# Kernel tuning notes

Hardware: AMD Instinct MI355X
Metric: run time of the kernel (lower is better)

The kernel has to match this reference:

```python
import jax, jax.numpy as jnp
import numpy as np

H = 12      # heads
P = 4       # dim_point
LN_EPS = 1e-5


def setup_inputs() -> dict:
    key = jax.random.key(0)
    ks = jax.random.split(key, 24)
    B, N, C, Dp, E = 1, 2048, 768, 128, 49152
    D3 = H * P * 3

    def w(k, shape, s=0.02):
        return jax.random.normal(k, shape, jnp.float32) * s

    inp = {
        'single': jax.random.normal(ks[0], (B, N, C), jnp.float32),
        'edge_feat': jax.random.normal(ks[1], (E, Dp), jnp.float32),
        'rot': jax.random.normal(ks[2], (B, N, 3, 3), jnp.float32),
        'trans': jax.random.normal(ks[3], (B, N, 3), jnp.float32),
        'Wq': w(ks[4], (C, C)), 'bq': jnp.zeros((C,), jnp.float32),
        'Wk': w(ks[5], (C, C)), 'bk': jnp.zeros((C,), jnp.float32),
        'Wv': w(ks[6], (C, C)), 'bv': jnp.zeros((C,), jnp.float32),
        'Wpb': w(ks[7], (Dp, H)), 'bpb': jnp.zeros((H,), jnp.float32),
        'Wqp': w(ks[8], (C, D3)), 'bqp': jnp.zeros((D3,), jnp.float32),
        'Wkp': w(ks[9], (C, D3)), 'bkp': jnp.zeros((D3,), jnp.float32),
        'Wvp': w(ks[10], (C, D3)), 'bvp': jnp.zeros((D3,), jnp.float32),
        'Wo': w(ks[11], (C, C)), 'bo': jnp.zeros((C,), jnp.float32),
        'Wpo': w(ks[12], (D3, C)), 'bpo': jnp.zeros((C,), jnp.float32),
        'gamma': jnp.ones((C,), jnp.float32),
        'beta': jnp.zeros((C,), jnp.float32),
        'edge_index': jax.random.randint(ks[13], (2, E), 0, B * N, jnp.int64),
    }
    return inp


def reference(single, edge_feat, rot, trans,
              Wq, bq, Wk, bk, Wv, bv, Wpb, bpb,
              Wqp, bqp, Wkp, bkp, Wvp, bvp,
              Wo, bo, Wpo, bpo, gamma, beta, edge_index):
    B, N, C = single.shape
    C_h = C // H
    scale = C_h ** (-0.5)

    # scalar q/k/v: [B,N,H,C_h]
    q = (single @ Wq + bq).reshape(B, N, H, C_h)
    k = (single @ Wk + bk).reshape(B, N, H, C_h)
    v = (single @ Wv + bv).reshape(B, N, H, C_h)

    # sparse pair bias scatter -> dense [B,H,N,N], symmetrized
    pbs = edge_feat @ Wpb + bpb                       # [E,H]
    src, dst = edge_index[0], edge_index[1]
    b_idx, ls, ld = src // N, src % N, dst % N
    pair_bias = jnp.zeros((B, H, N, N), single.dtype).at[b_idx, :, ls, ld].set(pbs)
    pair_bias = pair_bias + jnp.swapaxes(pair_bias, -1, -2)

    # point q/k/v in global frame: [B,N,H,P,3]
    def to_global(W, b):
        pts = (single @ W + b).reshape(B, N, H, P, 3)
        return jnp.einsum('bnhpd,bnde->bnhpe', pts, rot) + trans[:, :, None, None, :]

    q_pts = to_global(Wqp, bqp)
    k_pts = to_global(Wkp, bkp)
    v_pts = to_global(Wvp, bvp)

    q2 = jnp.sum(q_pts ** 2, axis=(3, 4))             # [B,N,H]
    k2 = jnp.sum(k_pts ** 2, axis=(3, 4))             # [B,N,H]

    # logits (blockwise loop in torch == full computation; math identical)
    scalar_logits = jnp.einsum('bqhc,bkhc->bhqk', q, k) * scale
    qk_pts = jnp.einsum('bqhpd,bkhpd->bhqk', q_pts, k_pts)
    point_logits = -0.5 * (jnp.transpose(q2, (0, 2, 1))[:, :, :, None]
                           + jnp.transpose(k2, (0, 2, 1))[:, :, None, :]
                           - 2.0 * qk_pts) * scale
    logits = scalar_logits + point_logits + pair_bias
    attn = jax.nn.softmax(logits, axis=-1)            # [B,H,N,N]

    attn_scalar = jnp.einsum('bhqk,bkhc->bqhc', attn, v).reshape(B, N, C)
    attn_points = jnp.einsum('bhqk,bkhpd->bqhpd', attn, v_pts).reshape(B, N, H * P * 3)

    out = (attn_scalar @ Wo + bo) + (attn_points @ Wpo + bpo)
    x = single + out
    mu = jnp.mean(x, axis=-1, keepdims=True)
    var = jnp.mean((x - mu) ** 2, axis=-1, keepdims=True)
    return (x - mu) * jax.lax.rsqrt(var + LN_EPS) * gamma + beta
```

## Files before the change

### kernel.cpp

```cpp
#include <hip/hip_runtime.h>

#define NRES 2048
#define NH 12
#define CDIM 768
#define NCVT 16
#define QKELEMS (NH * NRES * 96)
#define LOG2E 1.44269504f

typedef unsigned short u16;
typedef __bf16 bf16x8 __attribute__((ext_vector_type(8)));
typedef float f32x4 __attribute__((ext_vector_type(4)));

#define MFMA16(a,b,c) __builtin_amdgcn_mfma_f32_16x16x32_bf16(a,b,c,0,0,0)

__device__ __forceinline__ float bf2f(u16 u){
  unsigned int x = ((unsigned int)u) << 16;
  return __builtin_bit_cast(float, x);
}
__device__ __forceinline__ u16 f2bf(float f){
  unsigned int x = __builtin_bit_cast(unsigned int, f);
  x += 0x7fffu + ((x >> 16) & 1u);
  return (u16)(x >> 16);
}

__global__ void detect_kernel(const unsigned int* __restrict__ g,
                              const int* __restrict__ ei, int* __restrict__ flags)
{
  if (threadIdx.x == 0 && blockIdx.x == 0) {
    flags[0] = (g[0] == 0x3F800000u) ? 1 : 0;
    int allz = 1;
    for (int i = 1; i < 64; i += 2) allz &= (ei[i] == 0);
    flags[1] = allz;
  }
}

struct CvtDesc {
  const void* src[NCVT];
  void* dst[NCVT];
  int n[NCVT];
  int f32dst[NCVT];
  int nblk[NCVT];
};

__global__ __launch_bounds__(256) void cvt_kernel(CvtDesc d, const int* __restrict__ flags)
{
  int b = blockIdx.x, id = 0;
  while (id < NCVT - 1 && b >= d.nblk[id]) { b -= d.nblk[id]; id++; }
  int n = d.n[id];
  int base = (b * 256 + threadIdx.x) * 4;
  if (base >= n) return;
  int srcf32 = flags[0];
  const void* s = d.src[id];
  void* o = d.dst[id];
  int f32o = d.f32dst[id];
  #pragma unroll
  for (int k = 0; k < 4; k++) {
    int i = base + k;
    if (i >= n) break;
    float v = srcf32 ? ((const float*)s)[i] : bf2f(((const u16*)s)[i]);
    if (f32o) ((float*)o)[i] = v;
    else      ((u16*)o)[i] = f2bf(v);
  }
}

struct TDesc { const void* src; u16* dst; int R, C, ostride, ooff, rtiles, ctiles; };
struct TTable { TDesc d[9]; };

__global__ __launch_bounds__(256) void tcvt_kernel(TTable tt, const int* __restrict__ flags)
{
  TDesc d = tt.d[blockIdx.y];
  int tr = blockIdx.x % d.rtiles, tc = blockIdx.x / d.rtiles;
  if (tc >= d.ctiles) return;
  int srcf32 = flags[0];
  __shared__ float tile[32][33];
  int r0 = tr * 32, c0 = tc * 32;
  int x = threadIdx.x, y = threadIdx.y;
  #pragma unroll
  for (int i = 0; i < 32; i += 8) {
    int r = r0 + y + i, c = c0 + x;
    float v = 0.f;
    if (r < d.R && c < d.C) {
      long idx = (long)r * d.C + c;
      v = srcf32 ? ((const float*)d.src)[idx] : bf2f(((const u16*)d.src)[idx]);
    }
    tile[y + i][x] = v;
  }
  __syncthreads();
  #pragma unroll
  for (int i = 0; i < 32; i += 8) {
    int c = c0 + y + i, r = r0 + x;
    if (c < d.C && r < d.R) d.dst[(long)c * d.ostride + d.ooff + r] = f2bf(tile[x][y + i]);
  }
}

__global__ __launch_bounds__(256) void transpose_k(
    const u16* __restrict__ in, u16* __restrict__ out,
    int R, int Cc, int ostride, int ooff, long inBatch, long outBatch)
{
  in  += (long)blockIdx.z * inBatch;
  out += (long)blockIdx.z * outBatch;
  __shared__ u16 tile[32][33];
  int r0 = blockIdx.x * 32, c0 = blockIdx.y * 32;
  int tc = threadIdx.x, tr = threadIdx.y;
  #pragma unroll
  for (int i = 0; i < 32; i += 8) {
    int r = r0 + tr + i, c = c0 + tc;
    tile[tr + i][tc] = (r < R && c < Cc) ? in[(long)r * Cc + c] : (u16)0;
  }
  __syncthreads();
  #pragma unroll
  for (int i = 0; i < 32; i += 8) {
    int c = c0 + tr + i, r = r0 + tc;
    if (c < Cc && r < R) out[(long)c * ostride + ooff + r] = tile[tc][tr + i];
  }
}

__global__ __launch_bounds__(256) void scatter_kernel(
    const int* __restrict__ ei, const int* __restrict__ flags,
    int* __restrict__ winner, int* __restrict__ winnerT, int E)
{
  int e = blockIdx.x * 256 + threadIdx.x;
  if (e >= E) return;
  int s, d;
  if (flags[1]) { s = ei[2 * e]; d = ei[2 * (E + e)]; }
  else          { s = ei[e];     d = ei[E + e]; }
  int ls = s % NRES, ld = d % NRES;
  atomicMax(&winner[(long)ls * NRES + ld], e);
  atomicMax(&winnerT[(long)ld * NRES + ls], e);
}

__global__ __launch_bounds__(256) void bias_fill(
    const int* __restrict__ winner, const int* __restrict__ winnerT,
    const float* __restrict__ pbs, unsigned int* __restrict__ Bias)
{
  long idx = ((long)blockIdx.x * 256 + threadIdx.x) * 2;
  int2 w1 = *(const int2*)&winner[idx];
  int2 w2 = *(const int2*)&winnerT[idx];
  float b0[NH], b1[NH];
  #pragma unroll
  for (int h = 0; h < NH; h++) { b0[h] = 0.f; b1[h] = 0.f; }
  int ws0[2] = { w1.x, w2.x };
  int ws1[2] = { w1.y, w2.y };
  #pragma unroll
  for (int t = 0; t < 2; t++) {
    if (ws0[t] >= 0) {
      const float* p = &pbs[(long)ws0[t] * NH];
      #pragma unroll
      for (int h = 0; h < NH; h++) b0[h] += p[h];
    }
    if (ws1[t] >= 0) {
      const float* p = &pbs[(long)ws1[t] * NH];
      #pragma unroll
      for (int h = 0; h < NH; h++) b1[h] += p[h];
    }
  }
  long half = idx >> 1;
  #pragma unroll
  for (int h = 0; h < NH; h++) {
    unsigned int pack = (unsigned int)f2bf(b0[h] * LOG2E) | ((unsigned int)f2bf(b1[h] * LOG2E) << 16);
    Bias[(long)h * (NRES * (long)NRES / 2) + half] = pack;
  }
}

__global__ __launch_bounds__(256) void gemm64(
    const u16* __restrict__ A, int lda, const u16* __restrict__ BT, int ldb,
    const u16* __restrict__ bias1, const u16* __restrict__ bias2,
    const float* __restrict__ residf,
    int Nout, int Ktot, int mode, void* __restrict__ outp)
{
  __shared__ u16 As[64][40];
  __shared__ u16 Bs[64][40];
  int tid = threadIdx.x;
  int wave = tid >> 6, lane = tid & 63;
  int wr = (wave >> 1) * 32, wc = (wave & 1) * 32;
  int row0 = blockIdx.x * 64, col0 = blockIdx.y * 64;
  int rsub = lane & 15, kb8 = (lane >> 4) * 8;
  int sr = tid >> 2, sseg = tid & 3;
  f32x4 acc[2][2] = {};
  for (int k0 = 0; k0 < Ktot; k0 += 32) {
    __syncthreads();
    uint4 av = *(const uint4*)&A[(long)(row0 + sr) * lda + k0 + sseg * 8];
    *(uint4*)&As[sr][sseg * 8] = av;
    uint4 bv = {0u, 0u, 0u, 0u};
    if (col0 + sr < Nout) bv = *(const uint4*)&BT[(long)(col0 + sr) * ldb + k0 + sseg * 8];
    *(uint4*)&Bs[sr][sseg * 8] = bv;
    __syncthreads();
    bf16x8 af0 = *(const bf16x8*)&As[wr + rsub][kb8];
    bf16x8 af1 = *(const bf16x8*)&As[wr + 16 + rsub][kb8];
    bf16x8 bt0 = *(const bf16x8*)&Bs[wc + rsub][kb8];
    bf16x8 bt1 = *(const bf16x8*)&Bs[wc + 16 + rsub][kb8];
    acc[0][0] = MFMA16(af0, bt0, acc[0][0]);
    acc[0][1] = MFMA16(af0, bt1, acc[0][1]);
    acc[1][0] = MFMA16(af1, bt0, acc[1][0]);
    acc[1][1] = MFMA16(af1, bt1, acc[1][1]);
  }
  #pragma unroll
  for (int fm = 0; fm < 2; fm++)
  #pragma unroll
  for (int fn = 0; fn < 2; fn++)
  #pragma unroll
  for (int r = 0; r < 4; r++) {
    int row = row0 + wr + fm * 16 + (lane >> 4) * 4 + r;
    int col = col0 + wc + fn * 16 + rsub;
    if (col >= Nout) continue;
    float v = acc[fm][fn][r];
    if (mode == 1) {
      ((float*)outp)[(long)row * Nout + col] = v + bf2f(bias1[col]);
    } else if (mode == 2) {
      v += bf2f(bias1[col]) + bf2f(bias2[col]) + residf[(long)row * CDIM + col];
      ((float*)outp)[(long)row * CDIM + col] = v;
    } else {
      int seg = col / 768;
      int lc = col - seg * 768;
      int hh = lc >> 6, c6 = lc & 63;
      float sc = (seg == 0) ? (0.125f * LOG2E) : 1.0f;
      v = (v + bf2f(bias1[col])) * sc;
      u16* qb = (u16*)outp;
      u16* dst;
      if (seg < 2) dst = qb + (long)seg * QKELEMS + (long)hh * NRES * 96 + (long)row * 96 + c6;
      else         dst = qb + 2L * QKELEMS + (long)hh * NRES * 80 + (long)row * 80 + c6;
      *dst = f2bf(v);
    }
  }
}

__global__ __launch_bounds__(256) void point_transform(
    const float* __restrict__ Tmp3, const float* __restrict__ rot, const float* __restrict__ trans,
    u16* __restrict__ Qext, float* __restrict__ q2s, float* __restrict__ k2s)
{
  int t = blockIdx.x * 256 + threadIdx.x;
  if (t >= NRES * NH) return;
  int n = t / NH, h = t - n * NH;
  float R[9], T3[3];
  #pragma unroll
  for (int i = 0; i < 9; i++) R[i] = rot[n * 9 + i];
  #pragma unroll
  for (int i = 0; i < 3; i++) T3[i] = trans[n * 3 + i];
  #pragma unroll
  for (int seg = 0; seg < 3; seg++) {
    const float* lp = &Tmp3[(long)n * 432 + seg * 144 + h * 12];
    u16* dst;
    float scale;
    int npad;
    if (seg < 2) { dst = Qext + (long)seg * QKELEMS + (long)h * NRES * 96 + (long)n * 96 + 64; scale = (seg == 0) ? 0.125f * LOG2E : 1.0f; npad = 20; }
    else         { dst = Qext + 2L * QKELEMS + (long)h * NRES * 80 + (long)n * 80 + 64; scale = 1.0f; npad = 4; }
    float g2 = 0.f;
    #pragma unroll
    for (int pp = 0; pp < 4; pp++) {
      float a = lp[pp * 3], b = lp[pp * 3 + 1], c = lp[pp * 3 + 2];
      #pragma unroll
      for (int e = 0; e < 3; e++) {
        float g = a * R[e] + b * R[3 + e] + c * R[6 + e] + T3[e];
        g2 += g * g;
        dst[pp * 3 + e] = f2bf(scale * g);
      }
    }
    for (int p = 0; p < npad; p++) dst[12 + p] = 0;
    if (seg == 0) q2s[(long)h * NRES + n] = 0.0625f * LOG2E * g2;
    if (seg == 1) k2s[(long)h * NRES + n] = 0.0625f * LOG2E * g2;
  }
}

__global__ __launch_bounds__(256) void attn_pass1(
    const u16* __restrict__ Qext, const u16* __restrict__ VextT,
    const float* __restrict__ q2s, const float* __restrict__ k2s,
    const u16* __restrict__ Bias, float* __restrict__ Part)
{
  int h = blockIdx.y;
  int part = blockIdx.z;
  int q0 = blockIdx.x * 64;
  int tid = threadIdx.x, wave = tid >> 6, lane = tid & 63;
  int rsub = lane & 15, kb8 = (lane >> 4) * 8;
  __shared__ u16 Ks[32][104];
  __shared__ u16 Vs[80][40];
  __shared__ u16 Bs64[64][40];
  __shared__ u16 Ps[4][16][40];

  const u16* Qh = Qext + (long)h * NRES * 96;
  const u16* Kh = Qext + (long)QKELEMS + (long)h * NRES * 96;
  const u16* VTh = VextT + (long)h * 80 * NRES;
  const float* k2h = k2s + (long)h * NRES;
  const u16* BiasH = Bias + (long)h * NRES * NRES;

  int qrow = q0 + wave * 16;
  bf16x8 qf[3];
  #pragma unroll
  for (int f = 0; f < 3; f++)
    qf[f] = *(const bf16x8*)&Qh[(long)(qrow + rsub) * 96 + f * 32 + kb8];
  int crow = qrow + (lane >> 4) * 4;
  int lrow0 = wave * 16 + (lane >> 4) * 4;
  float q2r[4];
  #pragma unroll
  for (int r = 0; r < 4; r++) q2r[r] = q2s[(long)h * NRES + crow + r];
  float lsum[4] = {0.f, 0.f, 0.f, 0.f};
  f32x4 acc[5] = {};

  int jbase = part * 512;
  int krr = tid / 6, kcc = (tid - krr * 6) * 16;
  int vrr = tid >> 2, vcc = (tid & 3) * 8;
  uint4 kr0, kr1, vr0, vr1, br;

  auto LOAD = [&](int t) {
    int j0 = jbase + t * 32;
    if (tid < 192) {
      kr0 = *(const uint4*)&Kh[(long)(j0 + krr) * 96 + kcc];
      kr1 = *(const uint4*)&Kh[(long)(j0 + krr) * 96 + kcc + 8];
    }
    vr0 = *(const uint4*)&VTh[(long)vrr * NRES + j0 + vcc];
    if (tid < 64)
      vr1 = *(const uint4*)&VTh[(long)(64 + vrr) * NRES + j0 + vcc];
    br = *(const uint4*)&BiasH[(long)(q0 + vrr) * NRES + j0 + vcc];
  };

  LOAD(0);
  for (int t = 0; t < 16; t++) {
    int j0 = jbase + t * 32;
    __syncthreads();
    if (tid < 192) {
      *(uint4*)&Ks[krr][kcc]     = kr0;
      *(uint4*)&Ks[krr][kcc + 8] = kr1;
    }
    *(uint4*)&Vs[vrr][vcc] = vr0;
    if (tid < 64) *(uint4*)&Vs[64 + vrr][vcc] = vr1;
    *(uint4*)&Bs64[vrr][vcc] = br;
    __syncthreads();
    if (t < 15) LOAD(t + 1);

    f32x4 s[2];
    #pragma unroll
    for (int fn = 0; fn < 2; fn++) {
      f32x4 sv = {0.f, 0.f, 0.f, 0.f};
      #pragma unroll
      for (int f = 0; f < 3; f++) {
        bf16x8 kf = *(const bf16x8*)&Ks[fn * 16 + rsub][f * 32 + kb8];
        sv = MFMA16(qf[f], kf, sv);
      }
      s[fn] = sv;
    }
    #pragma unroll
    for (int fn = 0; fn < 2; fn++) {
      float k2v = k2h[j0 + fn * 16 + rsub];
      #pragma unroll
      for (int r = 0; r < 4; r++) {
        float b = bf2f(Bs64[lrow0 + r][fn * 16 + rsub]);
        float p = exp2f(s[fn][r] - q2r[r] - k2v + b);
        lsum[r] += p;
        Ps[wave][(lane >> 4) * 4 + r][fn * 16 + rsub] = f2bf(p);
      }
    }
    asm volatile("s_waitcnt lgkmcnt(0)" ::: "memory");
    __builtin_amdgcn_sched_barrier(0);
    bf16x8 pa = *(const bf16x8*)&Ps[wave][rsub][kb8];
    #pragma unroll
    for (int ff = 0; ff < 5; ff++) {
      bf16x8 vf = *(const bf16x8*)&Vs[ff * 16 + rsub][kb8];
      acc[ff] = MFMA16(pa, vf, acc[ff]);
    }
  }
  #pragma unroll
  for (int d = 1; d < 16; d <<= 1)
    #pragma unroll
    for (int r = 0; r < 4; r++) lsum[r] += __shfl_xor(lsum[r], d, 16);
  #pragma unroll
  for (int r = 0; r < 4; r++) {
    long basep = ((long)(part * NH + h) * NRES + (crow + r)) * 84;
    #pragma unroll
    for (int ff = 0; ff < 5; ff++)
      Part[basep + ff * 16 + rsub] = acc[ff][r];
    if (rsub == 0) Part[basep + 80] = lsum[r];
  }
}

__global__ __launch_bounds__(256) void attn_pass2(
    const float* __restrict__ Part, u16* __restrict__ ASP)
{
  int gid = blockIdx.x * 256 + threadIdx.x;
  int c = gid % 80;
  int pr = gid / 80;
  int h = pr / NRES, row = pr - h * NRES;
  float num = 0.f, den = 0.f;
  #pragma unroll
  for (int p = 0; p < 4; p++) {
    long basep = ((long)(p * NH + h) * NRES + row) * 84;
    num += Part[basep + c];
    den += Part[basep + 80];
  }
  float v = num / den;
  if (c < 64)      ASP[(long)row * 928 + h * 64 + c] = f2bf(v);
  else if (c < 76) ASP[(long)row * 928 + 768 + h * 12 + (c - 64)] = f2bf(v);
}

__global__ __launch_bounds__(256) void ln_kernel(
    const float* __restrict__ X, const float* __restrict__ gamma,
    const float* __restrict__ beta, const int* __restrict__ flags, void* __restrict__ out)
{
  int row = blockIdx.x;
  const float* x = &X[(long)row * CDIM];
  float s = 0.f, s2 = 0.f;
  for (int c = threadIdx.x; c < CDIM; c += 256) { float v = x[c]; s += v; s2 += v * v; }
  #pragma unroll
  for (int d = 1; d < 64; d <<= 1) { s += __shfl_xor(s, d, 64); s2 += __shfl_xor(s2, d, 64); }
  __shared__ float red[2][4];
  int wave = threadIdx.x >> 6, lane = threadIdx.x & 63;
  if (lane == 0) { red[0][wave] = s; red[1][wave] = s2; }
  __syncthreads();
  s = red[0][0] + red[0][1] + red[0][2] + red[0][3];
  s2 = red[1][0] + red[1][1] + red[1][2] + red[1][3];
  float mu = s * (1.f / CDIM);
  float var = s2 * (1.f / CDIM) - mu * mu;
  float rstd = rsqrtf(var + 1e-5f);
  int f32o = flags[0];
  for (int c = threadIdx.x; c < CDIM; c += 256) {
    float v = (x[c] - mu) * rstd * gamma[c] + beta[c];
    if (f32o) ((float*)out)[(long)row * CDIM + c] = v;
    else      ((u16*)out)[(long)row * CDIM + c] = f2bf(v);
  }
}

extern "C" void kernel_launch(void* const* d_in, const int* in_sizes, int n_in,
                              void* d_out, int out_size, void* d_ws, size_t ws_size,
                              hipStream_t stream)
{
  const void* single = d_in[0];
  const void* edge_feat = d_in[1];
  const void* rot = d_in[2];
  const void* trans = d_in[3];
  const void* Wq = d_in[4];  const void* bq = d_in[5];
  const void* Wk = d_in[6];  const void* bk = d_in[7];
  const void* Wv = d_in[8];  const void* bv = d_in[9];
  const void* Wpb = d_in[10]; const void* bpb = d_in[11];
  const void* Wqp = d_in[12]; const void* bqp = d_in[13];
  const void* Wkp = d_in[14]; const void* bkp = d_in[15];
  const void* Wvp = d_in[16]; const void* bvp = d_in[17];
  const void* Wo = d_in[18];  const void* bo = d_in[19];
  const void* Wpo = d_in[20]; const void* bpo = d_in[21];
  const void* gamma = d_in[22];
  const void* beta = d_in[23];
  const int* edge_index = (const int*)d_in[24];
  int E = in_sizes[24] / 2;

  char* base = (char*)d_ws;
  size_t off = 0;
  auto alloc = [&](size_t bytes) -> char* {
    char* r = base + off;
    off = (off + bytes + 255) & ~(size_t)255;
    return r;
  };
  int*   flags  = (int*)  alloc(256);
  int*   winner = (int*)  alloc((size_t)NRES * NRES * 4);
  int*   winnerT= (int*)  alloc((size_t)NRES * NRES * 4);
  u16*   Bias   = (u16*)  alloc((size_t)NH * NRES * NRES * 2);
  float* pbs    = (float*)alloc((size_t)E * NH * 4);
  float* Part   = (float*)winner;
  u16*   Qext   = (u16*)  alloc((size_t)QKELEMS * 2);
  u16*   Kext   = (u16*)  alloc((size_t)QKELEMS * 2);
  u16*   Vext   = (u16*)  alloc((size_t)NH * NRES * 80 * 2);
  u16*   VextT  = (u16*)  alloc((size_t)NH * 80 * NRES * 2);
  float* q2s    = (float*)alloc((size_t)NH * NRES * 4);
  float* k2s    = (float*)alloc((size_t)NH * NRES * 4);
  float* Tmp3   = (float*)alloc((size_t)NRES * 432 * 4);
  u16*   ASP    = (u16*)  alloc((size_t)NRES * 928 * 2);
  float* X      = (float*)alloc((size_t)NRES * CDIM * 4);
  u16* WqkvT = (u16*)alloc((size_t)2304 * 768 * 2);
  u16* WqkpT = (u16*)alloc((size_t)432 * 768 * 2);
  u16* WpbT  = (u16*)alloc((size_t)12 * 128 * 2);
  u16* WcatT = (u16*)alloc((size_t)768 * 928 * 2);
  u16*   single_bf  = (u16*)  alloc((size_t)NRES * 768 * 2);
  float* single_f32 = (float*)alloc((size_t)NRES * 768 * 4);
  u16*   ef_bf      = (u16*)  alloc((size_t)E * 128 * 2);
  float* rot_f      = (float*)alloc((size_t)NRES * 9 * 4);
  float* trans_f    = (float*)alloc((size_t)NRES * 3 * 4);
  u16* bqkv   = (u16*)alloc(2304*2);
  u16* bpb_bf = (u16*)alloc(12*2);
  u16* bqkp   = (u16*)alloc(432*2);
  u16* bo_bf  = (u16*)alloc(768*2);
  u16* bpo_bf = (u16*)alloc(768*2);
  float* gamma_f = (float*)alloc(768*4);
  float* beta_f  = (float*)alloc(768*4);

  hipMemsetAsync(winner,  0xFF, (size_t)NRES * NRES * 4, stream);
  hipMemsetAsync(winnerT, 0xFF, (size_t)NRES * NRES * 4, stream);
  hipMemsetAsync(ASP,  0, (size_t)NRES * 928 * 2, stream);
  hipMemsetAsync(WcatT,0, (size_t)768 * 928 * 2, stream);

  detect_kernel<<<1, 64, 0, stream>>>((const unsigned int*)gamma, edge_index, flags);

  CvtDesc cd;
  const void* srcs[NCVT] = { single, single, edge_feat, rot, trans,
    bq, bk, bv, bpb, bqp, bkp, bvp, bo, bpo, gamma, beta };
  void* dsts[NCVT] = { single_bf, single_f32, ef_bf, rot_f, trans_f,
    bqkv, bqkv + 768, bqkv + 1536, bpb_bf, bqkp, bqkp + 144, bqkp + 288,
    bo_bf, bpo_bf, gamma_f, beta_f };
  int ns[NCVT] = { NRES*768, NRES*768, E*128, NRES*9, NRES*3,
    768, 768, 768, 12, 144, 144, 144, 768, 768, 768, 768 };
  int f32d[NCVT] = { 0, 1, 0, 1, 1,
    0, 0, 0, 0, 0, 0, 0, 0, 0, 1, 1 };
  int totblk = 0;
  for (int i = 0; i < NCVT; i++) {
    cd.src[i]=srcs[i]; cd.dst[i]=dsts[i]; cd.n[i]=ns[i]; cd.f32dst[i]=f32d[i];
    cd.nblk[i] = (ns[i] + 1023) / 1024; totblk += cd.nblk[i];
  }
  cvt_kernel<<<totblk, 256, 0, stream>>>(cd, flags);

  TTable tt;
  auto setT = [&](int i, const void* s, u16* d, int R, int C, int ostride, int ooff) {
    tt.d[i] = TDesc{ s, d, R, C, ostride, ooff, (R + 31) / 32, (C + 31) / 32 };
  };
  setT(0, Wq,  WqkvT,             768, 768, 768, 0);
  setT(1, Wk,  WqkvT + 768*768,   768, 768, 768, 0);
  setT(2, Wv,  WqkvT + 2*768*768, 768, 768, 768, 0);
  setT(3, Wqp, WqkpT,             768, 144, 768, 0);
  setT(4, Wkp, WqkpT + 144*768,   768, 144, 768, 0);
  setT(5, Wvp, WqkpT + 288*768,   768, 144, 768, 0);
  setT(6, Wpb, WpbT,              128, 12,  128, 0);
  setT(7, Wo,  WcatT,             768, 768, 928, 0);
  setT(8, Wpo, WcatT,             144, 768, 928, 768);
  tcvt_kernel<<<dim3(576, 9), dim3(32, 8), 0, stream>>>(tt, flags);

  gemm64<<<dim3(E/64, 1), 256, 0, stream>>>(ef_bf, 128, WpbT, 128, bpb_bf, nullptr, nullptr, 12, 128, 1, pbs);
  scatter_kernel<<<(E + 255) / 256, 256, 0, stream>>>(edge_index, flags, winner, winnerT, E);
  bias_fill<<<(NRES * NRES / 2 + 255) / 256, 256, 0, stream>>>(winner, winnerT, pbs, (unsigned int*)Bias);

  gemm64<<<dim3(32, 36), 256, 0, stream>>>(single_bf, 768, WqkvT, 768, bqkv, nullptr, nullptr, 2304, 768, 3, Qext);
  gemm64<<<dim3(32, 7), 256, 0, stream>>>(single_bf, 768, WqkpT, 768, bqkp, nullptr, nullptr, 432, 768, 1, Tmp3);
  point_transform<<<(NRES * NH + 255) / 256, 256, 0, stream>>>(Tmp3, rot_f, trans_f, Qext, q2s, k2s);

  transpose_k<<<dim3(64,3,12), dim3(32,8), 0, stream>>>(Vext, VextT, NRES, 80, NRES, 0,
                                                        (long)NRES * 80, (long)80 * NRES);

  attn_pass1<<<dim3(32, 12, 4), 256, 0, stream>>>(Qext, VextT, q2s, k2s, Bias, Part);
  attn_pass2<<<(NRES * NH * 80) / 256, 256, 0, stream>>>(Part, ASP);

  gemm64<<<dim3(32, 12), 256, 0, stream>>>(ASP, 928, WcatT, 928, bo_bf, bpo_bf, single_f32, 768, 928, 2, X);

  ln_kernel<<<NRES, 256, 0, stream>>>(X, gamma_f, beta_f, flags, (u16*)d_out);
}
```

Baseline: 230.8 us.

## Fuse point projection into QKV GEMM and double-buffer attention prefetch

Result: faster. 213.0 us (-7.7%).

```diff
diff --git a/kernel.cpp b/kernel.cpp
--- a/kernel.cpp
+++ b/kernel.cpp
@@ -210,16 +210,20 @@
       v += bf2f(bias1[col]) + bf2f(bias2[col]) + residf[(long)row * CDIM + col];
       ((float*)outp)[(long)row * CDIM + col] = v;
     } else {
-      int seg = col / 768;
-      int lc = col - seg * 768;
-      int hh = lc >> 6, c6 = lc & 63;
-      float sc = (seg == 0) ? (0.125f * LOG2E) : 1.0f;
-      v = (v + bf2f(bias1[col])) * sc;
-      u16* qb = (u16*)outp;
-      u16* dst;
-      if (seg < 2) dst = qb + (long)seg * QKELEMS + (long)hh * NRES * 96 + (long)row * 96 + c6;
-      else         dst = qb + 2L * QKELEMS + (long)hh * NRES * 80 + (long)row * 80 + c6;
-      *dst = f2bf(v);
+      if (col < 2304) {
+        int seg = col / 768;
+        int lc = col - seg * 768;
+        int hh = lc >> 6, c6 = lc & 63;
+        float sc = (seg == 0) ? (0.125f * LOG2E) : 1.0f;
+        v = (v + bf2f(bias1[col])) * sc;
+        u16* qb = (u16*)outp;
+        u16* dst;
+        if (seg < 2) dst = qb + (long)seg * QKELEMS + (long)hh * NRES * 96 + (long)row * 96 + c6;
+        else         dst = qb + 2L * QKELEMS + (long)hh * NRES * 80 + (long)row * 80 + c6;
+        *dst = f2bf(v);
+      } else {
+        ((float*)residf)[(long)row * 432 + (col - 2304)] = v + bf2f(bias1[col]);
+      }
     }
   }
 }
@@ -298,65 +302,83 @@
   int jbase = part * 512;
   int krr = tid / 6, kcc = (tid - krr * 6) * 16;
   int vrr = tid >> 2, vcc = (tid & 3) * 8;
-  uint4 kr0, kr1, vr0, vr1, br;
-
-  auto LOAD = [&](int t) {
-    int j0 = jbase + t * 32;
-    if (tid < 192) {
-      kr0 = *(const uint4*)&Kh[(long)(j0 + krr) * 96 + kcc];
-      kr1 = *(const uint4*)&Kh[(long)(j0 + krr) * 96 + kcc + 8];
-    }
-    vr0 = *(const uint4*)&VTh[(long)vrr * NRES + j0 + vcc];
-    if (tid < 64)
-      vr1 = *(const uint4*)&VTh[(long)(64 + vrr) * NRES + j0 + vcc];
-    br = *(const uint4*)&BiasH[(long)(q0 + vrr) * NRES + j0 + vcc];
-  };
-
-  LOAD(0);
-  for (int t = 0; t < 16; t++) {
-    int j0 = jbase + t * 32;
+  uint4 kr0A, kr1A, vr0A, vr1A, brA;
+  uint4 kr0B, kr1B, vr0B, vr1B, brB;
+
+#define LOADSET(K0,K1,V0,V1,BR,T) do {                                         \
+    int j0_ = jbase + (T) * 32;                                                \
+    if (tid < 192) {                                                           \
+      K0 = *(const uint4*)&Kh[(long)(j0_ + krr) * 96 + kcc];                   \
+      K1 = *(const uint4*)&Kh[(long)(j0_ + krr) * 96 + kcc + 8];               \
+    }                                                                          \
+    V0 = *(const uint4*)&VTh[(long)vrr * NRES + j0_ + vcc];                    \
+    if (tid < 64)                                                              \
+      V1 = *(const uint4*)&VTh[(long)(64 + vrr) * NRES + j0_ + vcc];           \
+    BR = *(const uint4*)&BiasH[(long)(q0 + vrr) * NRES + j0_ + vcc];           \
+  } while (0)
+
+#define WRITESET(K0,K1,V0,V1,BR) do {                                          \
+    if (tid < 192) {                                                           \
+      *(uint4*)&Ks[krr][kcc]     = K0;                                         \
+      *(uint4*)&Ks[krr][kcc + 8] = K1;                                         \
+    }                                                                          \
+    *(uint4*)&Vs[vrr][vcc] = V0;                                               \
+    if (tid < 64) *(uint4*)&Vs[64 + vrr][vcc] = V1;                            \
+    *(uint4*)&Bs64[vrr][vcc] = BR;                                             \
+  } while (0)
+
+#define COMPUTE(T) do {                                                        \
+    int j0_ = jbase + (T) * 32;                                                \
+    f32x4 s[2];                                                                \
+    _Pragma("unroll")                                                          \
+    for (int fn = 0; fn < 2; fn++) {                                           \
+      f32x4 sv = {0.f, 0.f, 0.f, 0.f};                                         \
+      _Pragma("unroll")                                                        \
+      for (int f = 0; f < 3; f++) {                                            \
+        bf16x8 kf = *(const bf16x8*)&Ks[fn * 16 + rsub][f * 32 + kb8];         \
+        sv = MFMA16(qf[f], kf, sv);                                            \
+      }                                                                        \
+      s[fn] = sv;                                                              \
+    }                                                                          \
+    _Pragma("unroll")                                                          \
+    for (int fn = 0; fn < 2; fn++) {                                           \
+      float k2v = k2h[j0_ + fn * 16 + rsub];                                   \
+      _Pragma("unroll")                                                        \
+      for (int r = 0; r < 4; r++) {                                            \
+        float b = bf2f(Bs64[lrow0 + r][fn * 16 + rsub]);                       \
+        float p = exp2f(s[fn][r] - q2r[r] - k2v + b);                          \
+        lsum[r] += p;                                                          \
+        Ps[wave][(lane >> 4) * 4 + r][fn * 16 + rsub] = f2bf(p);               \
+      }                                                                        \
+    }                                                                          \
+    asm volatile("s_waitcnt lgkmcnt(0)" ::: "memory");                         \
+    __builtin_amdgcn_sched_barrier(0);                                         \
+    bf16x8 pa = *(const bf16x8*)&Ps[wave][rsub][kb8];                          \
+    _Pragma("unroll")                                                          \
+    for (int ff = 0; ff < 5; ff++) {                                           \
+      bf16x8 vf = *(const bf16x8*)&Vs[ff * 16 + rsub][kb8];                    \
+      acc[ff] = MFMA16(pa, vf, acc[ff]);                                       \
+    }                                                                          \
+  } while (0)
+
+  LOADSET(kr0A, kr1A, vr0A, vr1A, brA, 0);
+  LOADSET(kr0B, kr1B, vr0B, vr1B, brB, 1);
+  for (int t = 0; t < 16; t += 2) {
     __syncthreads();
-    if (tid < 192) {
-      *(uint4*)&Ks[krr][kcc]     = kr0;
-      *(uint4*)&Ks[krr][kcc + 8] = kr1;
-    }
-    *(uint4*)&Vs[vrr][vcc] = vr0;
-    if (tid < 64) *(uint4*)&Vs[64 + vrr][vcc] = vr1;
-    *(uint4*)&Bs64[vrr][vcc] = br;
+    WRITESET(kr0A, kr1A, vr0A, vr1A, brA);
     __syncthreads();
-    if (t < 15) LOAD(t + 1);
-
-    f32x4 s[2];
-    #pragma unroll
-    for (int fn = 0; fn < 2; fn++) {
-      f32x4 sv = {0.f, 0.f, 0.f, 0.f};
-      #pragma unroll
-      for (int f = 0; f < 3; f++) {
-        bf16x8 kf = *(const bf16x8*)&Ks[fn * 16 + rsub][f * 32 + kb8];
-        sv = MFMA16(qf[f], kf, sv);
-      }
-      s[fn] = sv;
-    }
-    #pragma unroll
-    for (int fn = 0; fn < 2; fn++) {
-      float k2v = k2h[j0 + fn * 16 + rsub];
-      #pragma unroll
-      for (int r = 0; r < 4; r++) {
-        float b = bf2f(Bs64[lrow0 + r][fn * 16 + rsub]);
-        float p = exp2f(s[fn][r] - q2r[r] - k2v + b);
-        lsum[r] += p;
-        Ps[wave][(lane >> 4) * 4 + r][fn * 16 + rsub] = f2bf(p);
-      }
-    }
-    asm volatile("s_waitcnt lgkmcnt(0)" ::: "memory");
-    __builtin_amdgcn_sched_barrier(0);
-    bf16x8 pa = *(const bf16x8*)&Ps[wave][rsub][kb8];
-    #pragma unroll
-    for (int ff = 0; ff < 5; ff++) {
-      bf16x8 vf = *(const bf16x8*)&Vs[ff * 16 + rsub][kb8];
-      acc[ff] = MFMA16(pa, vf, acc[ff]);
-    }
-  }
+    if (t + 2 < 16) LOADSET(kr0A, kr1A, vr0A, vr1A, brA, t + 2);
+    COMPUTE(t);
+    __syncthreads();
+    WRITESET(kr0B, kr1B, vr0B, vr1B, brB);
+    __syncthreads();
+    if (t + 3 < 16) LOADSET(kr0B, kr1B, vr0B, vr1B, brB, t + 3);
+    COMPUTE(t + 1);
+  }
+#undef LOADSET
+#undef WRITESET
+#undef COMPUTE
+
   #pragma unroll
   for (int d = 1; d < 16; d <<= 1)
     #pragma unroll
@@ -461,8 +483,7 @@
   float* Tmp3   = (float*)alloc((size_t)NRES * 432 * 4);
   u16*   ASP    = (u16*)  alloc((size_t)NRES * 928 * 2);
   float* X      = (float*)alloc((size_t)NRES * CDIM * 4);
-  u16* WqkvT = (u16*)alloc((size_t)2304 * 768 * 2);
-  u16* WqkpT = (u16*)alloc((size_t)432 * 768 * 2);
+  u16* WqkvT = (u16*)alloc((size_t)2736 * 768 * 2);
   u16* WpbT  = (u16*)alloc((size_t)12 * 128 * 2);
   u16* WcatT = (u16*)alloc((size_t)768 * 928 * 2);
   u16*   single_bf  = (u16*)  alloc((size_t)NRES * 768 * 2);
@@ -470,18 +491,15 @@
   u16*   ef_bf      = (u16*)  alloc((size_t)E * 128 * 2);
   float* rot_f      = (float*)alloc((size_t)NRES * 9 * 4);
   float* trans_f    = (float*)alloc((size_t)NRES * 3 * 4);
-  u16* bqkv   = (u16*)alloc(2304*2);
+  u16* bqkvp  = (u16*)alloc(2736*2);
   u16* bpb_bf = (u16*)alloc(12*2);
-  u16* bqkp   = (u16*)alloc(432*2);
   u16* bo_bf  = (u16*)alloc(768*2);
   u16* bpo_bf = (u16*)alloc(768*2);
   float* gamma_f = (float*)alloc(768*4);
   float* beta_f  = (float*)alloc(768*4);
 
-  hipMemsetAsync(winner,  0xFF, (size_t)NRES * NRES * 4, stream);
-  hipMemsetAsync(winnerT, 0xFF, (size_t)NRES * NRES * 4, stream);
-  hipMemsetAsync(ASP,  0, (size_t)NRES * 928 * 2, stream);
-  hipMemsetAsync(WcatT,0, (size_t)768 * 928 * 2, stream);
+  hipMemsetAsync(winner, 0xFF, (size_t)NRES * NRES * 8, stream);
+  hipMemsetAsync(WcatT, 0, (size_t)768 * 928 * 2, stream);
 
   detect_kernel<<<1, 64, 0, stream>>>((const unsigned int*)gamma, edge_index, flags);
 
@@ -489,7 +507,7 @@
   const void* srcs[NCVT] = { single, single, edge_feat, rot, trans,
     bq, bk, bv, bpb, bqp, bkp, bvp, bo, bpo, gamma, beta };
   void* dsts[NCVT] = { single_bf, single_f32, ef_bf, rot_f, trans_f,
-    bqkv, bqkv + 768, bqkv + 1536, bpb_bf, bqkp, bqkp + 144, bqkp + 288,
+    bqkvp, bqkvp + 768, bqkvp + 1536, bpb_bf, bqkvp + 2304, bqkvp + 2448, bqkvp + 2592,
     bo_bf, bpo_bf, gamma_f, beta_f };
   int ns[NCVT] = { NRES*768, NRES*768, E*128, NRES*9, NRES*3,
     768, 768, 768, 12, 144, 144, 144, 768, 768, 768, 768 };
@@ -509,9 +527,9 @@
   setT(0, Wq,  WqkvT,             768, 768, 768, 0);
   setT(1, Wk,  WqkvT + 768*768,   768, 768, 768, 0);
   setT(2, Wv,  WqkvT + 2*768*768, 768, 768, 768, 0);
-  setT(3, Wqp, WqkpT,             768, 144, 768, 0);
-  setT(4, Wkp, WqkpT + 144*768,   768, 144, 768, 0);
-  setT(5, Wvp, WqkpT + 288*768,   768, 144, 768, 0);
+  setT(3, Wqp, WqkvT + 2304*768,  768, 144, 768, 0);
+  setT(4, Wkp, WqkvT + 2448*768,  768, 144, 768, 0);
+  setT(5, Wvp, WqkvT + 2592*768,  768, 144, 768, 0);
   setT(6, Wpb, WpbT,              128, 12,  128, 0);
   setT(7, Wo,  WcatT,             768, 768, 928, 0);
   setT(8, Wpo, WcatT,             144, 768, 928, 768);
@@ -521,8 +539,7 @@
   scatter_kernel<<<(E + 255) / 256, 256, 0, stream>>>(edge_index, flags, winner, winnerT, E);
   bias_fill<<<(NRES * NRES / 2 + 255) / 256, 256, 0, stream>>>(winner, winnerT, pbs, (unsigned int*)Bias);
 
-  gemm64<<<dim3(32, 36), 256, 0, stream>>>(single_bf, 768, WqkvT, 768, bqkv, nullptr, nullptr, 2304, 768, 3, Qext);
-  gemm64<<<dim3(32, 7), 256, 0, stream>>>(single_bf, 768, WqkpT, 768, bqkp, nullptr, nullptr, 432, 768, 1, Tmp3);
+  gemm64<<<dim3(32, 43), 256, 0, stream>>>(single_bf, 768, WqkvT, 768, bqkvp, nullptr, Tmp3, 2736, 768, 3, Qext);
   point_transform<<<(NRES * NH + 255) / 256, 256, 0, stream>>>(Tmp3, rot_f, trans_f, Qext, q2s, k2s);
 
   transpose_k<<<dim3(64,3,12), dim3(32,8), 0, stream>>>(Vext, VextT, NRES, 80, NRES, 0,
```

## Store pair bias as 8-bit float, fuse point GEMM, fold row sums into MFMA

Applied to the files above, without the earlier changes.

Result: faster. 223.0 us (-3.4%).

```diff
diff --git a/kernel.cpp b/kernel.cpp
--- a/kernel.cpp
+++ b/kernel.cpp
@@ -8,6 +8,7 @@
 #define LOG2E 1.44269504f
 
 typedef unsigned short u16;
+typedef unsigned char u8;
 typedef __bf16 bf16x8 __attribute__((ext_vector_type(8)));
 typedef float f32x4 __attribute__((ext_vector_type(4)));
 
@@ -21,6 +22,28 @@
   unsigned int x = __builtin_bit_cast(unsigned int, f);
   x += 0x7fffu + ((x >> 16) & 1u);
   return (u16)(x >> 16);
+}
+
+__device__ __forceinline__ unsigned int enc8(float f){
+  if (f == 0.f) return 0u;
+  unsigned int bits = __builtin_bit_cast(unsigned int, f);
+  unsigned int s = (bits >> 24) & 0x80u;
+  unsigned int a = bits & 0x7fffffffu;
+  if (a >= 0x3C800000u) {
+    a += 0x0007FFFFu + ((a >> 20) & 1u);
+    if (a > 0x43E00000u) a = 0x43E00000u;
+    return s | (((a >> 23) - 120u) << 3) | ((a >> 20) & 7u);
+  }
+  float av = __builtin_bit_cast(float, a);
+  unsigned int q = (unsigned int)(av * 512.f + 0.5f);
+  if (q > 7u) return s | 0x08u;
+  return s | q;
+}
+__device__ __forceinline__ float dec8(unsigned int b){
+  unsigned int e = (b >> 3) & 15u, m = b & 7u;
+  float v = (e == 0) ? (float)m * 0.001953125f
+                     : __builtin_bit_cast(float, ((e + 120u) << 23) | (m << 20));
+  return (b & 0x80u) ? -v : v;
 }
 
 __global__ void detect_kernel(const unsigned int* __restrict__ g,
@@ -131,34 +154,39 @@
 
 __global__ __launch_bounds__(256) void bias_fill(
     const int* __restrict__ winner, const int* __restrict__ winnerT,
-    const float* __restrict__ pbs, unsigned int* __restrict__ Bias)
-{
-  long idx = ((long)blockIdx.x * 256 + threadIdx.x) * 2;
-  int2 w1 = *(const int2*)&winner[idx];
-  int2 w2 = *(const int2*)&winnerT[idx];
-  float b0[NH], b1[NH];
-  #pragma unroll
-  for (int h = 0; h < NH; h++) { b0[h] = 0.f; b1[h] = 0.f; }
-  int ws0[2] = { w1.x, w2.x };
-  int ws1[2] = { w1.y, w2.y };
-  #pragma unroll
-  for (int t = 0; t < 2; t++) {
-    if (ws0[t] >= 0) {
-      const float* p = &pbs[(long)ws0[t] * NH];
+    const float* __restrict__ pbs, unsigned int* __restrict__ Bias8)
+{
+  long idx = ((long)blockIdx.x * 256 + threadIdx.x) * 4;
+  int4 w1 = *(const int4*)&winner[idx];
+  int4 w2 = *(const int4*)&winnerT[idx];
+  float b[4][NH];
+  #pragma unroll
+  for (int c = 0; c < 4; c++)
+    #pragma unroll
+    for (int h = 0; h < NH; h++) b[c][h] = 0.f;
+  int wa[4] = { w1.x, w1.y, w1.z, w1.w };
+  int wb[4] = { w2.x, w2.y, w2.z, w2.w };
+  #pragma unroll
+  for (int c = 0; c < 4; c++) {
+    if (wa[c] >= 0) {
+      const float* p = &pbs[(long)wa[c] * NH];
       #pragma unroll
-      for (int h = 0; h < NH; h++) b0[h] += p[h];
-    }
-    if (ws1[t] >= 0) {
-      const float* p = &pbs[(long)ws1[t] * NH];
+      for (int h = 0; h < NH; h++) b[c][h] += p[h];
+    }
+    if (wb[c] >= 0) {
+      const float* p = &pbs[(long)wb[c] * NH];
       #pragma unroll
-      for (int h = 0; h < NH; h++) b1[h] += p[h];
-    }
-  }
-  long half = idx >> 1;
+      for (int h = 0; h < NH; h++) b[c][h] += p[h];
+    }
+  }
+  long quarter = idx >> 2;
   #pragma unroll
   for (int h = 0; h < NH; h++) {
-    unsigned int pack = (unsigned int)f2bf(b0[h] * LOG2E) | ((unsigned int)f2bf(b1[h] * LOG2E) << 16);
-    Bias[(long)h * (NRES * (long)NRES / 2) + half] = pack;
+    unsigned int pack = enc8(b[0][h] * LOG2E)
+                      | (enc8(b[1][h] * LOG2E) << 8)
+                      | (enc8(b[2][h] * LOG2E) << 16)
+                      | (enc8(b[3][h] * LOG2E) << 24);
+    Bias8[(long)h * (NRES * (long)NRES / 4) + quarter] = pack;
   }
 }
 
@@ -210,16 +238,20 @@
       v += bf2f(bias1[col]) + bf2f(bias2[col]) + residf[(long)row * CDIM + col];
       ((float*)outp)[(long)row * CDIM + col] = v;
     } else {
-      int seg = col / 768;
-      int lc = col - seg * 768;
-      int hh = lc >> 6, c6 = lc & 63;
-      float sc = (seg == 0) ? (0.125f * LOG2E) : 1.0f;
-      v = (v + bf2f(bias1[col])) * sc;
-      u16* qb = (u16*)outp;
-      u16* dst;
-      if (seg < 2) dst = qb + (long)seg * QKELEMS + (long)hh * NRES * 96 + (long)row * 96 + c6;
-      else         dst = qb + 2L * QKELEMS + (long)hh * NRES * 80 + (long)row * 80 + c6;
-      *dst = f2bf(v);
+      if (col < 2304) {
+        int seg = col / 768;
+        int lc = col - seg * 768;
+        int hh = lc >> 6, c6 = lc & 63;
+        float sc = (seg == 0) ? (0.125f * LOG2E) : 1.0f;
+        v = (v + bf2f(bias1[col])) * sc;
+        u16* qb = (u16*)outp;
+        u16* dst;
+        if (seg < 2) dst = qb + (long)seg * QKELEMS + (long)hh * NRES * 96 + (long)row * 96 + c6;
+        else         dst = qb + 2L * QKELEMS + (long)hh * NRES * 80 + (long)row * 80 + c6;
+        *dst = f2bf(v);
+      } else {
+        ((float*)residf)[(long)row * 432 + (col - 2304)] = v + bf2f(bias1[col]);
+      }
     }
   }
 }
@@ -264,7 +296,7 @@
 __global__ __launch_bounds__(256) void attn_pass1(
     const u16* __restrict__ Qext, const u16* __restrict__ VextT,
     const float* __restrict__ q2s, const float* __restrict__ k2s,
-    const u16* __restrict__ Bias, float* __restrict__ Part)
+    const u8* __restrict__ Bias8, float* __restrict__ Part)
 {
   int h = blockIdx.y;
   int part = blockIdx.z;
@@ -272,15 +304,20 @@
   int tid = threadIdx.x, wave = tid >> 6, lane = tid & 63;
   int rsub = lane & 15, kb8 = (lane >> 4) * 8;
   __shared__ u16 Ks[32][104];
-  __shared__ u16 Vs[80][40];
-  __shared__ u16 Bs64[64][40];
+  __shared__ u16 Vs[96][40];
+  __shared__ __align__(16) u8 Bs64[64][32];
   __shared__ u16 Ps[4][16][40];
 
   const u16* Qh = Qext + (long)h * NRES * 96;
   const u16* Kh = Qext + (long)QKELEMS + (long)h * NRES * 96;
   const u16* VTh = VextT + (long)h * 80 * NRES;
   const float* k2h = k2s + (long)h * NRES;
-  const u16* BiasH = Bias + (long)h * NRES * NRES;
+  const u8* BiasH = Bias8 + (long)h * NRES * NRES;
+
+  for (int u = tid; u < 16 * 32; u += 256) {
+    int rr = 80 + (u >> 5), cc = u & 31;
+    Vs[rr][cc] = (rr == 80) ? (u16)0x3F80 : (u16)0;
+  }
 
   int qrow = q0 + wave * 16;
   bf16x8 qf[3];
@@ -292,12 +329,12 @@
   float q2r[4];
   #pragma unroll
   for (int r = 0; r < 4; r++) q2r[r] = q2s[(long)h * NRES + crow + r];
-  float lsum[4] = {0.f, 0.f, 0.f, 0.f};
-  f32x4 acc[5] = {};
+  f32x4 acc[6] = {};
 
   int jbase = part * 512;
   int krr = tid / 6, kcc = (tid - krr * 6) * 16;
   int vrr = tid >> 2, vcc = (tid & 3) * 8;
+  int brow = tid >> 1, bseg = (tid & 1) * 16;
   uint4 kr0, kr1, vr0, vr1, br;
 
   auto LOAD = [&](int t) {
@@ -309,7 +346,8 @@
     vr0 = *(const uint4*)&VTh[(long)vrr * NRES + j0 + vcc];
     if (tid < 64)
       vr1 = *(const uint4*)&VTh[(long)(64 + vrr) * NRES + j0 + vcc];
-    br = *(const uint4*)&BiasH[(long)(q0 + vrr) * NRES + j0 + vcc];
+    if (tid < 128)
+      br = *(const uint4*)&BiasH[(long)(q0 + brow) * NRES + j0 + bseg];
   };
 
   LOAD(0);
@@ -322,7 +360,7 @@
     }
     *(uint4*)&Vs[vrr][vcc] = vr0;
     if (tid < 64) *(uint4*)&Vs[64 + vrr][vcc] = vr1;
-    *(uint4*)&Bs64[vrr][vcc] = br;
+    if (tid < 128) *(uint4*)&Bs64[brow][bseg] = br;
     __syncthreads();
     if (t < 15) LOAD(t + 1);
 
@@ -342,9 +380,8 @@
       float k2v = k2h[j0 + fn * 16 + rsub];
       #pragma unroll
       for (int r = 0; r < 4; r++) {
-        float b = bf2f(Bs64[lrow0 + r][fn * 16 + rsub]);
+        float b = dec8(Bs64[lrow0 + r][fn * 16 + rsub]);
         float p = exp2f(s[fn][r] - q2r[r] - k2v + b);
-        lsum[r] += p;
         Ps[wave][(lane >> 4) * 4 + r][fn * 16 + rsub] = f2bf(p);
       }
     }
@@ -352,22 +389,18 @@
     __builtin_amdgcn_sched_barrier(0);
     bf16x8 pa = *(const bf16x8*)&Ps[wave][rsub][kb8];
     #pragma unroll
-    for (int ff = 0; ff < 5; ff++) {
+    for (int ff = 0; ff < 6; ff++) {
       bf16x8 vf = *(const bf16x8*)&Vs[ff * 16 + rsub][kb8];
       acc[ff] = MFMA16(pa, vf, acc[ff]);
     }
   }
-  #pragma unroll
-  for (int d = 1; d < 16; d <<= 1)
-    #pragma unroll
-    for (int r = 0; r < 4; r++) lsum[r] += __shfl_xor(lsum[r], d, 16);
   #pragma unroll
   for (int r = 0; r < 4; r++) {
     long basep = ((long)(part * NH + h) * NRES + (crow + r)) * 84;
     #pragma unroll
     for (int ff = 0; ff < 5; ff++)
       Part[basep + ff * 16 + rsub] = acc[ff][r];
-    if (rsub == 0) Part[basep + 80] = lsum[r];
+    if (rsub == 0) Part[basep + 80] = acc[5][r];
   }
 }
 
@@ -449,7 +482,7 @@
   int*   flags  = (int*)  alloc(256);
   int*   winner = (int*)  alloc((size_t)NRES * NRES * 4);
   int*   winnerT= (int*)  alloc((size_t)NRES * NRES * 4);
-  u16*   Bias   = (u16*)  alloc((size_t)NH * NRES * NRES * 2);
+  u8*    Bias8  = (u8*)   alloc((size_t)NH * NRES * NRES);
   float* pbs    = (float*)alloc((size_t)E * NH * 4);
   float* Part   = (float*)winner;
   u16*   Qext   = (u16*)  alloc((size_t)QKELEMS * 2);
@@ -461,8 +494,7 @@
   float* Tmp3   = (float*)alloc((size_t)NRES * 432 * 4);
   u16*   ASP    = (u16*)  alloc((size_t)NRES * 928 * 2);
   float* X      = (float*)alloc((size_t)NRES * CDIM * 4);
-  u16* WqkvT = (u16*)alloc((size_t)2304 * 768 * 2);
-  u16* WqkpT = (u16*)alloc((size_t)432 * 768 * 2);
+  u16* WqkvT = (u16*)alloc((size_t)2736 * 768 * 2);
   u16* WpbT  = (u16*)alloc((size_t)12 * 128 * 2);
   u16* WcatT = (u16*)alloc((size_t)768 * 928 * 2);
   u16*   single_bf  = (u16*)  alloc((size_t)NRES * 768 * 2);
@@ -470,18 +502,15 @@
   u16*   ef_bf      = (u16*)  alloc((size_t)E * 128 * 2);
   float* rot_f      = (float*)alloc((size_t)NRES * 9 * 4);
   float* trans_f    = (float*)alloc((size_t)NRES * 3 * 4);
-  u16* bqkv   = (u16*)alloc(2304*2);
+  u16* bqkvp  = (u16*)alloc(2736*2);
   u16* bpb_bf = (u16*)alloc(12*2);
-  u16* bqkp   = (u16*)alloc(432*2);
   u16* bo_bf  = (u16*)alloc(768*2);
   u16* bpo_bf = (u16*)alloc(768*2);
   float* gamma_f = (float*)alloc(768*4);
   float* beta_f  = (float*)alloc(768*4);
 
-  hipMemsetAsync(winner,  0xFF, (size_t)NRES * NRES * 4, stream);
-  hipMemsetAsync(winnerT, 0xFF, (size_t)NRES * NRES * 4, stream);
-  hipMemsetAsync(ASP,  0, (size_t)NRES * 928 * 2, stream);
-  hipMemsetAsync(WcatT,0, (size_t)768 * 928 * 2, stream);
+  hipMemsetAsync(winner, 0xFF, (size_t)NRES * NRES * 8, stream);
+  hipMemsetAsync(WcatT, 0, (size_t)768 * 928 * 2, stream);
 
   detect_kernel<<<1, 64, 0, stream>>>((const unsigned int*)gamma, edge_index, flags);
 
@@ -489,7 +518,7 @@
   const void* srcs[NCVT] = { single, single, edge_feat, rot, trans,
     bq, bk, bv, bpb, bqp, bkp, bvp, bo, bpo, gamma, beta };
   void* dsts[NCVT] = { single_bf, single_f32, ef_bf, rot_f, trans_f,
-    bqkv, bqkv + 768, bqkv + 1536, bpb_bf, bqkp, bqkp + 144, bqkp + 288,
+    bqkvp, bqkvp + 768, bqkvp + 1536, bpb_bf, bqkvp + 2304, bqkvp + 2448, bqkvp + 2592,
     bo_bf, bpo_bf, gamma_f, beta_f };
   int ns[NCVT] = { NRES*768, NRES*768, E*128, NRES*9, NRES*3,
     768, 768, 768, 12, 144, 144, 144, 768, 768, 768, 768 };
@@ -509,9 +538,9 @@
   setT(0, Wq,  WqkvT,             768, 768, 768, 0);
   setT(1, Wk,  WqkvT + 768*768,   768, 768, 768, 0);
   setT(2, Wv,  WqkvT + 2*768*768, 768, 768, 768, 0);
-  setT(3, Wqp, WqkpT,             768, 144, 768, 0);
-  setT(4, Wkp, WqkpT + 144*768,   768, 144, 768, 0);
-  setT(5, Wvp, WqkpT + 288*768,   768, 144, 768, 0);
+  setT(3, Wqp, WqkvT + 2304*768,  768, 144, 768, 0);
+  setT(4, Wkp, WqkvT + 2448*768,  768, 144, 768, 0);
+  setT(5, Wvp, WqkvT + 2592*768,  768, 144, 768, 0);
   setT(6, Wpb, WpbT,              128, 12,  128, 0);
   setT(7, Wo,  WcatT,             768, 768, 928, 0);
   setT(8, Wpo, WcatT,             144, 768, 928, 768);
@@ -519,16 +548,15 @@
 
   gemm64<<<dim3(E/64, 1), 256, 0, stream>>>(ef_bf, 128, WpbT, 128, bpb_bf, nullptr, nullptr, 12, 128, 1, pbs);
   scatter_kernel<<<(E + 255) / 256, 256, 0, stream>>>(edge_index, flags, winner, winnerT, E);
-  bias_fill<<<(NRES * NRES / 2 + 255) / 256, 256, 0, stream>>>(winner, winnerT, pbs, (unsigned int*)Bias);
-
-  gemm64<<<dim3(32, 36), 256, 0, stream>>>(single_bf, 768, WqkvT, 768, bqkv, nullptr, nullptr, 2304, 768, 3, Qext);
-  gemm64<<<dim3(32, 7), 256, 0, stream>>>(single_bf, 768, WqkpT, 768, bqkp, nullptr, nullptr, 432, 768, 1, Tmp3);
+  bias_fill<<<(NRES * NRES / 4) / 256, 256, 0, stream>>>(winner, winnerT, pbs, (unsigned int*)Bias8);
+
+  gemm64<<<dim3(32, 43), 256, 0, stream>>>(single_bf, 768, WqkvT, 768, bqkvp, nullptr, Tmp3, 2736, 768, 3, Qext);
   point_transform<<<(NRES * NH + 255) / 256, 256, 0, stream>>>(Tmp3, rot_f, trans_f, Qext, q2s, k2s);
 
   transpose_k<<<dim3(64,3,12), dim3(32,8), 0, stream>>>(Vext, VextT, NRES, 80, NRES, 0,
                                                         (long)NRES * 80, (long)80 * NRES);
 
-  attn_pass1<<<dim3(32, 12, 4), 256, 0, stream>>>(Qext, VextT, q2s, k2s, Bias, Part);
+  attn_pass1<<<dim3(32, 12, 4), 256, 0, stream>>>(Qext, VextT, q2s, k2s, Bias8, Part);
   attn_pass2<<<(NRES * NH * 80) / 256, 256, 0, stream>>>(Part, ASP);
 
   gemm64<<<dim3(32, 12), 256, 0, stream>>>(ASP, 928, WcatT, 928, bo_bf, bpo_bf, single_f32, 768, 928, 2, X);
```
